# Optimization experiments

Measured on AMD Instinct MI355X. Metric: run time of the kernel, lower is better.

Reference implementation:

```python
import jax, jax.numpy as jnp
import numpy as np
import math

B, T, E, H, L, V = 256, 256, 64, 8, 6, 65
HS = E // H  # head_size = 8


def _pos_encoding():
    position = jnp.arange(T, dtype=jnp.float32)[:, None]
    div_term = jnp.exp(jnp.arange(0, E, 2, dtype=jnp.float32) * (-(math.log(10000.0) / E)))
    pe = jnp.zeros((T, E), dtype=jnp.float32)
    pe = pe.at[:, 0::2].set(jnp.sin(position * div_term))
    pe = pe.at[:, 1::2].set(jnp.cos(position * div_term))
    return pe


def _layernorm(x, g, b, eps=1e-5):
    mu = jnp.mean(x, axis=-1, keepdims=True)
    var = jnp.var(x, axis=-1, keepdims=True)
    return (x - mu) * jax.lax.rsqrt(var + eps) * g + b


def setup_inputs() -> dict:
    key = jax.random.key(0)
    ks = jax.random.split(key, 20)
    s = 0.02
    return {
        "inputs": jax.random.randint(ks[0], (B, T), 0, V),
        "labels": jax.random.randint(ks[1], (B, T), 0, V),
        "emb": jax.random.normal(ks[2], (V, E), jnp.float32) * s,
        "Wq": jax.random.normal(ks[3], (L, E, E), jnp.float32) * s,
        "bq": jnp.zeros((L, E), jnp.float32),
        "Wk": jax.random.normal(ks[4], (L, E, E), jnp.float32) * s,
        "bk": jnp.zeros((L, E), jnp.float32),
        "Wv": jax.random.normal(ks[5], (L, E, E), jnp.float32) * s,
        "bv": jnp.zeros((L, E), jnp.float32),
        "Wo": jax.random.normal(ks[6], (L, E, E), jnp.float32) * s,
        "bo": jnp.zeros((L, E), jnp.float32),
        "ln1_g": jnp.ones((L, E), jnp.float32),
        "ln1_b": jnp.zeros((L, E), jnp.float32),
        "ln2_g": jnp.ones((L, E), jnp.float32),
        "ln2_b": jnp.zeros((L, E), jnp.float32),
        "W1": jax.random.normal(ks[7], (L, E, 4 * E), jnp.float32) * s,
        "b1": jnp.zeros((L, 4 * E), jnp.float32),
        "W2": jax.random.normal(ks[8], (L, 4 * E, E), jnp.float32) * s,
        "b2": jnp.zeros((L, E), jnp.float32),
        "Wout": jax.random.normal(ks[9], (E, V), jnp.float32) * s,
        "bout": jnp.zeros((V,), jnp.float32),
    }


def reference(inputs, labels, emb, Wq, bq, Wk, bk, Wv, bv, Wo, bo,
              ln1_g, ln1_b, ln2_g, ln2_b, W1, b1, W2, b2, Wout, bout):
    x = emb[inputs] + _pos_encoding()[None, :, :]  # [B,T,E]
    causal = jnp.triu(jnp.ones((T, T), dtype=bool), k=1)  # True above diagonal -> masked
    scale = 1.0 / jnp.sqrt(jnp.float32(HS))
    for l in range(L):
        q = (x @ Wq[l] + bq[l]).reshape(B, T, H, HS)
        k = (x @ Wk[l] + bk[l]).reshape(B, T, H, HS)
        v = (x @ Wv[l] + bv[l]).reshape(B, T, H, HS)
        scores = jnp.einsum('bqhd,bkhd->bhqk', q, k) * scale  # [B,H,T,T]
        scores = jnp.where(causal, jnp.float32(-1e9), scores)
        attn = jax.nn.softmax(scores, axis=-1)
        o = jnp.einsum('bhqk,bkhd->bqhd', attn, v).reshape(B, T, E)
        x = _layernorm(x + (o @ Wo[l] + bo[l]), ln1_g[l], ln1_b[l])
        ff = jax.nn.relu(x @ W1[l] + b1[l]) @ W2[l] + b2[l]
        x = _layernorm(x + ff, ln2_g[l], ln2_b[l])
    logits = (x @ Wout + bout).reshape(B * T, V)
    logp = jax.nn.log_softmax(logits, axis=-1)
    loss = -jnp.mean(jnp.take_along_axis(logp, labels.reshape(B * T, 1), axis=-1))
    return logits, loss
```

## Files before the change

### kernel.cpp

```cpp
#include <hip/hip_runtime.h>
#include <math.h>

#define VOCAB 65
#define NBATCH 256

typedef __attribute__((ext_vector_type(8))) short bf16x8;
typedef __attribute__((ext_vector_type(4))) float f32x4;

#define MFMA16(a, b, c) __builtin_amdgcn_mfma_f32_16x16x32_bf16((a), (b), (c), 0, 0, 0)

__device__ __forceinline__ unsigned short f2b(float f) {
    union { float f; unsigned u; } v; v.f = f;
    unsigned r = (v.u + 0x7fffu + ((v.u >> 16) & 1u)) >> 16;
    return (unsigned short)r;
}
__device__ __forceinline__ unsigned cvtpk(float lo, float hi) {
    unsigned r; asm("v_cvt_pk_bf16_f32 %0, %1, %2" : "=v"(r) : "v"(lo), "v"(hi)); return r;
}
__device__ __forceinline__ unsigned short f2b1(float v) { return (unsigned short)cvtpk(v, v); }
__device__ __forceinline__ float b2f(unsigned short h) {
    union { unsigned u; float f; } v; v.u = ((unsigned)h) << 16; return v.f;
}
__device__ __forceinline__ float lo2f(unsigned wd) {
    union { unsigned u; float f; } v; v.u = wd << 16; return v.f;
}
__device__ __forceinline__ float hi2f(unsigned wd) {
    union { unsigned u; float f; } v; v.u = wd & 0xffff0000u; return v.f;
}

__global__ __launch_bounds__(256)
void prep_kernel(const float* __restrict__ Wq, const float* __restrict__ Wk,
                 const float* __restrict__ Wv, const float* __restrict__ Wo,
                 const float* __restrict__ W1, const float* __restrict__ W2,
                 const float* __restrict__ Wout, unsigned short* __restrict__ wbuf) {
    int l = blockIdx.y;
    int idx = blockIdx.x * 256 + threadIdx.x;
    if (l < 6) {
        float v; unsigned short* dst;
        if (idx < 12288) {
            int mat = idx >> 12, m = (idx >> 6) & 63, k = idx & 63;
            const float* W = mat == 0 ? Wq : (mat == 1 ? Wk : Wv);
            v = W[l * 4096 + k * 64 + m];
            dst = wbuf + l * 12288 + idx;
        } else if (idx < 16384) {
            int j = idx - 12288; int m = j >> 6, k = j & 63;
            v = Wo[l * 4096 + k * 64 + m];
            dst = wbuf + 73728 + l * 4096 + j;
        } else if (idx < 32768) {
            int j = idx - 16384; int m = j >> 6, k = j & 63;
            v = W1[l * 16384 + k * 256 + m];
            dst = wbuf + 98304 + l * 16384 + j;
        } else {
            int j = idx - 32768; int m = j >> 8, k = j & 255;
            v = W2[l * 16384 + k * 64 + m];
            dst = wbuf + 196608 + l * 16384 + j;
        }
        *dst = f2b(v);
    } else {
        if (idx < 5120) {
            int m = idx >> 6, k = idx & 63;
            float v = (m < 65) ? Wout[k * 65 + m] : 0.f;
            wbuf[294912 + idx] = f2b(v);
        } else if (idx < 21504) {
            int j = idx - 5120; int t = j >> 6, e = j & 63;
            int i2 = e >> 1;
            float div = expf(-(float)(2 * i2) * 0.14391156831212788f);
            float ang = (float)t * div;
            ((float*)(wbuf + 300032))[j] = (e & 1) ? cosf(ang) : sinf(ang);
        }
    }
}

__global__ __launch_bounds__(512)
void tf_kernel(const int* __restrict__ inp, const int* __restrict__ labels,
               const float* __restrict__ emb,
               const float* __restrict__ bq, const float* __restrict__ bk,
               const float* __restrict__ bv, const float* __restrict__ bo,
               const float* __restrict__ ln1g, const float* __restrict__ ln1b,
               const float* __restrict__ ln2g, const float* __restrict__ ln2b,
               const float* __restrict__ b1, const float* __restrict__ b2,
               const float* __restrict__ bout,
               const unsigned short* __restrict__ wbuf,
               float* __restrict__ out_logits, float* __restrict__ partials) {
    __shared__ __attribute__((aligned(16))) char smem[106528];
    unsigned short (*xb)[72]      = (unsigned short (*)[72])(smem);
    unsigned short (*q2)[24]      = (unsigned short (*)[24])(smem + 36864);
    unsigned short (*k2)[24]      = (unsigned short (*)[24])(smem + 49152);
    unsigned short (*vt)[264]     = (unsigned short (*)[264])(smem + 61440);
    unsigned short (*pcb)[16][40] = (unsigned short (*)[16][40])(smem + 69888);
    unsigned short (*proj)[72]    = (unsigned short (*)[72])(smem + 36864);
    unsigned short (*hb)[136]     = (unsigned short (*)[136])(smem + 36864);
    float* red = (float*)(smem + 106496);

    const unsigned short* wqkvt = wbuf;
    const unsigned short* wot   = wbuf + 73728;
    const unsigned short* w1t   = wbuf + 98304;
    const unsigned short* w2t   = wbuf + 196608;
    const unsigned short* woutt = wbuf + 294912;
    const float* pef = (const float*)(wbuf + 300032);

    const int b = blockIdx.x;
    const int tid = threadIdx.x;
    const int w = tid >> 6;
    const int lane = tid & 63;
    const int cc = lane & 15;
    const int gg = lane >> 4;

    const bf16x8 zf = {0, 0, 0, 0, 0, 0, 0, 0};
    const bf16x8 ones = {(short)0x3F80, (short)0x3F80, (short)0x3F80, (short)0x3F80,
                         (short)0x3F80, (short)0x3F80, (short)0x3F80, (short)0x3F80};

    unsigned rr[16];
    const int lrow = tid >> 1, lq = tid & 1;

    {
        int id = inp[b * 256 + lrow];
        const float4* er = (const float4*)(emb + id * 64 + 32 * lq);
        const float4* pr = (const float4*)(pef + lrow * 64 + 32 * lq);
        #pragma unroll
        for (int j = 0; j < 8; ++j) {
            float4 ev = er[j], pv = pr[j];
            rr[2 * j]     = cvtpk(ev.x + pv.x, ev.y + pv.y);
            rr[2 * j + 1] = cvtpk(ev.z + pv.z, ev.w + pv.w);
        }
        #pragma unroll
        for (int j = 0; j < 4; ++j)
            *(uint4*)&xb[lrow][32 * lq + 8 * j] = make_uint4(rr[4 * j], rr[4 * j + 1], rr[4 * j + 2], rr[4 * j + 3]);
    }
    __syncthreads();

    auto ownerLN = [&](const float* gp_, const float* bp_) {
        unsigned pw[16];
        #pragma unroll
        for (int j = 0; j < 4; ++j) {
            uint4 p = *(const uint4*)&proj[lrow][32 * lq + 8 * j];
            pw[4 * j] = p.x; pw[4 * j + 1] = p.y; pw[4 * j + 2] = p.z; pw[4 * j + 3] = p.w;
        }
        float xv[32];
        float s = 0.f, s2 = 0.f;
        #pragma unroll
        for (int j = 0; j < 16; ++j) {
            float x0 = lo2f(rr[j]) + lo2f(pw[j]);
            float x1 = hi2f(rr[j]) + hi2f(pw[j]);
            xv[2 * j] = x0; xv[2 * j + 1] = x1;
            s += x0 + x1; s2 += x0 * x0 + x1 * x1;
        }
        s  += __shfl_xor(s, 1, 64);
        s2 += __shfl_xor(s2, 1, 64);
        float mu = s * 0.015625f;
        float var = s2 * 0.015625f - mu * mu;
        float rstd = rsqrtf(var + 1e-5f);
        const float4* gp = (const float4*)(gp_ + 32 * lq);
        const float4* bp = (const float4*)(bp_ + 32 * lq);
        #pragma unroll
        for (int j = 0; j < 8; ++j) {
            float4 gv = gp[j], bv2 = bp[j];
            float n0 = (xv[4 * j]     - mu) * rstd * gv.x + bv2.x;
            float n1 = (xv[4 * j + 1] - mu) * rstd * gv.y + bv2.y;
            float n2 = (xv[4 * j + 2] - mu) * rstd * gv.z + bv2.z;
            float n3 = (xv[4 * j + 3] - mu) * rstd * gv.w + bv2.w;
            rr[2 * j]     = cvtpk(n0, n1);
            rr[2 * j + 1] = cvtpk(n2, n3);
        }
        #pragma unroll
        for (int j = 0; j < 4; ++j)
            *(uint4*)&xb[lrow][32 * lq + 8 * j] = make_uint4(rr[4 * j], rr[4 * j + 1], rr[4 * j + 2], rr[4 * j + 3]);
    };

    for (int l = 0; l < 6; ++l) {
        const unsigned short* Wqkv = wqkvt + l * 12288;

        bf16x8 af00 = *(const bf16x8*)&xb[16 * (2 * w)     + cc][8 * gg];
        bf16x8 af01 = *(const bf16x8*)&xb[16 * (2 * w)     + cc][32 + 8 * gg];
        bf16x8 af10 = *(const bf16x8*)&xb[16 * (2 * w + 1) + cc][8 * gg];
        bf16x8 af11 = *(const bf16x8*)&xb[16 * (2 * w + 1) + cc][32 + 8 * gg];

        #pragma unroll
        for (int p = 0; p < 4; ++p) {
            __syncthreads();
            #pragma unroll
            for (int mat = 0; mat < 3; ++mat) {
                const unsigned short* Wt = Wqkv + mat * 4096;
                bf16x8 bf0 = *(const bf16x8*)&Wt[(16 * p + cc) * 64 + 8 * gg];
                bf16x8 bf1 = *(const bf16x8*)&Wt[(16 * p + cc) * 64 + 32 + 8 * gg];
                const float* bias = (mat == 0 ? bq : (mat == 1 ? bk : bv)) + l * 64;
                float bb = bias[16 * p + cc];
                #pragma unroll
                for (int mi = 0; mi < 2; ++mi) {
                    int mt = 2 * w + mi;
                    f32x4 c = {0.f, 0.f, 0.f, 0.f};
                    c = MFMA16(mi ? af10 : af00, bf0, c);
                    c = MFMA16(mi ? af11 : af01, bf1, c);
                    if (mat == 0) {
                        #pragma unroll
                        for (int r = 0; r < 4; ++r)
                            q2[16 * mt + 4 * gg + r][cc] = f2b1((c[r] + bb) * 0.35355339059327373f);
                    } else if (mat == 1) {
                        #pragma unroll
                        for (int r = 0; r < 4; ++r)
                            k2[16 * mt + 4 * gg + r][cc] = f2b1(c[r] + bb);
                    } else {
                        uint2 pk;
                        pk.x = cvtpk(c[0] + bb, c[1] + bb);
                        pk.y = cvtpk(c[2] + bb, c[3] + bb);
                        *(uint2*)&vt[cc][16 * mt + 4 * gg] = pk;
                    }
                }
            }
            __syncthreads();

            #pragma unroll
            for (int hh = 0; hh < 2; ++hh) {
                const int h = 2 * p + hh;
                const int hoff = 8 * hh;
                int a_ = (w + h) & 7;
                #pragma unroll
                for (int s = 0; s < 2; ++s) {
                    int i = s ? (15 - a_) : a_;
                    bf16x8 qf = zf;
                    if (gg == 0) qf = *(const bf16x8*)&q2[16 * i + cc][hoff];
                    f32x4 o = {0.f, 0.f, 0.f, 0.f};
                    int full = i >> 1;
                    for (int jc = 0; jc < full; ++jc) {
                        #pragma unroll
                        for (int jt2 = 0; jt2 < 2; ++jt2) {
                            int jt = 2 * jc + jt2;
                            bf16x8 kf = zf;
                            if (gg == 0) kf = *(const bf16x8*)&k2[16 * jt + cc][hoff];
                            f32x4 sc = {0.f, 0.f, 0.f, 0.f};
                            sc = MFMA16(kf, qf, sc);
                            uint2 pk;
                            pk.x = cvtpk(__expf(sc[0]), __expf(sc[1]));
                            pk.y = cvtpk(__expf(sc[2]), __expf(sc[3]));
                            *(uint2*)&pcb[w][cc][16 * jt2 + 4 * gg] = pk;
                        }
                        asm volatile("" ::: "memory");
                        bf16x8 pa = *(const bf16x8*)&pcb[w][cc][8 * gg];
                        bf16x8 vb;
                        if (cc < 8)       vb = *(const bf16x8*)&vt[hoff + cc][32 * jc + 8 * gg];
                        else if (cc == 8) vb = ones;
                        else              vb = zf;
                        o = MFMA16(pa, vb, o);
                        asm volatile("" ::: "memory");
                    }
                    {
                        int jc = full;
                        #pragma unroll
                        for (int jt2 = 0; jt2 < 2; ++jt2) {
                            int jt = 2 * jc + jt2;
                            uint2 pk = make_uint2(0u, 0u);
                            if (jt <= i) {
                                bf16x8 kf = zf;
                                if (gg == 0) kf = *(const bf16x8*)&k2[16 * jt + cc][hoff];
                                f32x4 sc = {0.f, 0.f, 0.f, 0.f};
                                sc = MFMA16(kf, qf, sc);
                                float pv[4];
                                #pragma unroll
                                for (int r = 0; r < 4; ++r) {
                                    float pp = __expf(sc[r]);
                                    if (jt == i && 4 * gg + r > cc) pp = 0.f;
                                    pv[r] = pp;
                                }
                                pk.x = cvtpk(pv[0], pv[1]);
                                pk.y = cvtpk(pv[2], pv[3]);
                            }
                            *(uint2*)&pcb[w][cc][16 * jt2 + 4 * gg] = pk;
                        }
                        asm volatile("" ::: "memory");
                        bf16x8 pa = *(const bf16x8*)&pcb[w][cc][8 * gg];
                        bf16x8 vb;
                        if (cc < 8)       vb = *(const bf16x8*)&vt[hoff + cc][32 * jc + 8 * gg];
                        else if (cc == 8) vb = ones;
                        else              vb = zf;
                        o = MFMA16(pa, vb, o);
                        asm volatile("" ::: "memory");
                    }
                    #pragma unroll
                    for (int r = 0; r < 4; ++r) {
                        float rs = __shfl(o[r], (lane & 48) + 8, 64);
                        float ov = o[r] * __builtin_amdgcn_rcpf(rs);
                        if (cc < 8)
                            xb[16 * i + 4 * gg + r][8 * h + cc] = f2b1(ov);
                    }
                }
            }
        }
        __syncthreads();

        {
            const unsigned short* Wt = wot + l * 4096;
            int n = w & 3;
            bf16x8 bf0 = *(const bf16x8*)&Wt[(16 * n + cc) * 64 + 8 * gg];
            bf16x8 bf1 = *(const bf16x8*)&Wt[(16 * n + cc) * 64 + 32 + 8 * gg];
            float bb = bo[l * 64 + 16 * n + cc];
            #pragma unroll
            for (int mi = 0; mi < 8; ++mi) {
                int mt = 8 * (w >> 2) + mi;
                bf16x8 o0 = *(const bf16x8*)&xb[16 * mt + cc][8 * gg];
                bf16x8 o1 = *(const bf16x8*)&xb[16 * mt + cc][32 + 8 * gg];
                f32x4 c = {0.f, 0.f, 0.f, 0.f};
                c = MFMA16(o0, bf0, c);
                c = MFMA16(o1, bf1, c);
                #pragma unroll
                for (int r = 0; r < 4; ++r)
                    proj[16 * mt + 4 * gg + r][16 * n + cc] = f2b1(c[r] + bb);
            }
        }
        __syncthreads();
        ownerLN(ln1g + l * 64, ln1b + l * 64);
        __syncthreads();

        f32x4 facc[8];
        #pragma unroll
        for (int t = 0; t < 8; ++t) facc[t] = {0.f, 0.f, 0.f, 0.f};
        #pragma unroll
        for (int ch = 0; ch < 2; ++ch) {
            if (ch) __syncthreads();
            {
                const unsigned short* Wt = w1t + l * 16384;
                int gcol = 128 * ch + 16 * w + cc;
                bf16x8 bf0 = *(const bf16x8*)&Wt[gcol * 64 + 8 * gg];
                bf16x8 bf1 = *(const bf16x8*)&Wt[gcol * 64 + 32 + 8 * gg];
                float bb = b1[l * 256 + gcol];
                #pragma unroll
                for (int mt = 0; mt < 16; ++mt) {
                    bf16x8 x0 = *(const bf16x8*)&xb[16 * mt + cc][8 * gg];
                    bf16x8 x1 = *(const bf16x8*)&xb[16 * mt + cc][32 + 8 * gg];
                    f32x4 c = {0.f, 0.f, 0.f, 0.f};
                    c = MFMA16(x0, bf0, c);
                    c = MFMA16(x1, bf1, c);
                    #pragma unroll
                    for (int r = 0; r < 4; ++r)
                        hb[16 * mt + 4 * gg + r][16 * w + cc] = f2b1(fmaxf(c[r] + bb, 0.f));
                }
            }
            __syncthreads();
            {
                const unsigned short* Wt = w2t + l * 16384;
                int n = w & 3;
                #pragma unroll
                for (int ks = 0; ks < 4; ++ks) {
                    bf16x8 bf0 = *(const bf16x8*)&Wt[(16 * n + cc) * 256 + 128 * ch + 32 * ks + 8 * gg];
                    #pragma unroll
                    for (int mi = 0; mi < 8; ++mi) {
                        int mt = 8 * (w >> 2) + mi;
                        bf16x8 h0 = *(const bf16x8*)&hb[16 * mt + cc][32 * ks + 8 * gg];
                        facc[mi] = MFMA16(h0, bf0, facc[mi]);
                    }
                }
            }
        }
        __syncthreads();
        {
            int n = w & 3;
            float bb = b2[l * 64 + 16 * n + cc];
            #pragma unroll
            for (int mi = 0; mi < 8; ++mi) {
                int mt = 8 * (w >> 2) + mi;
                #pragma unroll
                for (int r = 0; r < 4; ++r)
                    proj[16 * mt + 4 * gg + r][16 * n + cc] = f2b1(facc[mi][r] + bb);
            }
        }
        __syncthreads();
        ownerLN(ln2g + l * 64, ln2b + l * 64);
        __syncthreads();
    }

    #pragma unroll
    for (int t = 0; t < 10; ++t) {
        int id = w + 8 * t;
        int n = id >> 4, mt = id & 15;
        bf16x8 a0 = *(const bf16x8*)&xb[16 * mt + cc][8 * gg];
        bf16x8 a1 = *(const bf16x8*)&xb[16 * mt + cc][32 + 8 * gg];
        bf16x8 bf0 = *(const bf16x8*)&woutt[(16 * n + cc) * 64 + 8 * gg];
        bf16x8 bf1 = *(const bf16x8*)&woutt[(16 * n + cc) * 64 + 32 + 8 * gg];
        f32x4 c = {0.f, 0.f, 0.f, 0.f};
        c = MFMA16(a0, bf0, c);
        c = MFMA16(a1, bf1, c);
        int col = 16 * n + cc;
        if (col < 65) {
            float bb = bout[col];
            #pragma unroll
            for (int r = 0; r < 4; ++r) {
                int row = 16 * mt + 4 * gg + r;
                float v = c[r] + bb;
                out_logits[((size_t)b * 256 + row) * 65 + col] = v;
                proj[row][col] = f2b1(v);
            }
        }
    }
    __syncthreads();

    {
        float sum = 0.f;
        for (int c2 = lq; c2 < 65; c2 += 2) sum += __expf(b2f(proj[lrow][c2]));
        sum += __shfl_xor(sum, 1, 64);
        float nll = 0.f;
        if (lq == 0) {
            int lab = labels[b * 256 + lrow];
            nll = logf(sum) - b2f(proj[lrow][lab]);
        }
        #pragma unroll
        for (int m = 1; m < 64; m <<= 1) nll += __shfl_xor(nll, m, 64);
        if (lane == 0) red[w] = nll;
        __syncthreads();
        if (tid == 0) {
            float s = 0.f;
            #pragma unroll
            for (int i = 0; i < 8; ++i) s += red[i];
            partials[b] = s;
        }
    }
}

__global__ __launch_bounds__(64)
void loss_reduce(const float* __restrict__ partials, float* __restrict__ out) {
    int t = threadIdx.x;
    float s = partials[t] + partials[t + 64] + partials[t + 128] + partials[t + 192];
    #pragma unroll
    for (int m = 1; m < 64; m <<= 1) s += __shfl_xor(s, m, 64);
    if (t == 0) out[0] = s * (1.f / 65536.f);
}

extern "C" void kernel_launch(void* const* d_in, const int* in_sizes, int n_in,
                              void* d_out, int out_size, void* d_ws, size_t ws_size,
                              hipStream_t stream) {
    const int*   inputs = (const int*)d_in[0];
    const int*   labels = (const int*)d_in[1];
    const float* emb  = (const float*)d_in[2];
    const float* Wq   = (const float*)d_in[3];
    const float* bq   = (const float*)d_in[4];
    const float* Wk   = (const float*)d_in[5];
    const float* bk   = (const float*)d_in[6];
    const float* Wv   = (const float*)d_in[7];
    const float* bv   = (const float*)d_in[8];
    const float* Wo   = (const float*)d_in[9];
    const float* bo   = (const float*)d_in[10];
    const float* ln1g = (const float*)d_in[11];
    const float* ln1b = (const float*)d_in[12];
    const float* ln2g = (const float*)d_in[13];
    const float* ln2b = (const float*)d_in[14];
    const float* W1   = (const float*)d_in[15];
    const float* b1   = (const float*)d_in[16];
    const float* W2   = (const float*)d_in[17];
    const float* b2   = (const float*)d_in[18];
    const float* Wout = (const float*)d_in[19];
    const float* bout = (const float*)d_in[20];

    float* logits = (float*)d_out;
    float* loss   = logits + (size_t)65536 * 65;

    float* partials = (float*)d_ws;
    unsigned short* wbuf = (unsigned short*)((char*)d_ws + 1024);

    prep_kernel<<<dim3(192, 7), 256, 0, stream>>>(Wq, Wk, Wv, Wo, W1, W2, Wout, wbuf);
    tf_kernel<<<NBATCH, 512, 0, stream>>>(inputs, labels, emb,
                                          bq, bk, bv, bo,
                                          ln1g, ln1b, ln2g, ln2b,
                                          b1, b2, bout,
                                          wbuf, logits, partials);
    loss_reduce<<<1, 64, 0, stream>>>(partials, loss);
}
```

Baseline: 309.7 us.

## Process four heads per QKV phase and double-chunk attention inner loop

QKV projection now produces 32 columns (four heads) per phase instead of 16, halving the number of projection/attention phases and block-wide barriers per layer. The attention inner loop processes two 32-key chunks per iteration into separate accumulators, so the score MFMAs and exp work of two chunks can overlap before the P·V MFMAs. This also merges the full-chunk and diagonal-chunk paths into one masked path. The cost is more LDS (larger q/k/v/pcb buffers), extra masking checks on every chunk, and more register pressure.

```diff
diff --git a/kernel.cpp b/kernel.cpp
--- a/kernel.cpp
+++ b/kernel.cpp
@@ -82,15 +82,15 @@
                const float* __restrict__ bout,
                const unsigned short* __restrict__ wbuf,
                float* __restrict__ out_logits, float* __restrict__ partials) {
-    __shared__ __attribute__((aligned(16))) char smem[106528];
+    __shared__ __attribute__((aligned(16))) char smem[113184];
     unsigned short (*xb)[72]      = (unsigned short (*)[72])(smem);
-    unsigned short (*q2)[24]      = (unsigned short (*)[24])(smem + 36864);
-    unsigned short (*k2)[24]      = (unsigned short (*)[24])(smem + 49152);
-    unsigned short (*vt)[264]     = (unsigned short (*)[264])(smem + 61440);
-    unsigned short (*pcb)[16][40] = (unsigned short (*)[16][40])(smem + 69888);
+    unsigned short (*q2)[40]      = (unsigned short (*)[40])(smem + 36864);
+    unsigned short (*k2)[40]      = (unsigned short (*)[40])(smem + 57344);
+    unsigned short (*vt)[264]     = (unsigned short (*)[264])(smem + 77824);
+    unsigned short (*pcb)[16][72] = (unsigned short (*)[16][72])(smem + 94720);
     unsigned short (*proj)[72]    = (unsigned short (*)[72])(smem + 36864);
     unsigned short (*hb)[136]     = (unsigned short (*)[136])(smem + 36864);
-    float* red = (float*)(smem + 106496);
+    float* red = (float*)(smem + 113152);
 
     const unsigned short* wqkvt = wbuf;
     const unsigned short* wot   = wbuf + 73728;
@@ -176,82 +176,64 @@
         bf16x8 af11 = *(const bf16x8*)&xb[16 * (2 * w + 1) + cc][32 + 8 * gg];
 
         #pragma unroll
-        for (int p = 0; p < 4; ++p) {
-            __syncthreads();
-            #pragma unroll
-            for (int mat = 0; mat < 3; ++mat) {
-                const unsigned short* Wt = Wqkv + mat * 4096;
-                bf16x8 bf0 = *(const bf16x8*)&Wt[(16 * p + cc) * 64 + 8 * gg];
-                bf16x8 bf1 = *(const bf16x8*)&Wt[(16 * p + cc) * 64 + 32 + 8 * gg];
-                const float* bias = (mat == 0 ? bq : (mat == 1 ? bk : bv)) + l * 64;
-                float bb = bias[16 * p + cc];
-                #pragma unroll
-                for (int mi = 0; mi < 2; ++mi) {
-                    int mt = 2 * w + mi;
-                    f32x4 c = {0.f, 0.f, 0.f, 0.f};
-                    c = MFMA16(mi ? af10 : af00, bf0, c);
-                    c = MFMA16(mi ? af11 : af01, bf1, c);
-                    if (mat == 0) {
-                        #pragma unroll
-                        for (int r = 0; r < 4; ++r)
-                            q2[16 * mt + 4 * gg + r][cc] = f2b1((c[r] + bb) * 0.35355339059327373f);
-                    } else if (mat == 1) {
-                        #pragma unroll
-                        for (int r = 0; r < 4; ++r)
-                            k2[16 * mt + 4 * gg + r][cc] = f2b1(c[r] + bb);
-                    } else {
-                        uint2 pk;
-                        pk.x = cvtpk(c[0] + bb, c[1] + bb);
-                        pk.y = cvtpk(c[2] + bb, c[3] + bb);
-                        *(uint2*)&vt[cc][16 * mt + 4 * gg] = pk;
+        for (int ph = 0; ph < 2; ++ph) {
+            if (ph) __syncthreads();
+            #pragma unroll
+            for (int lp = 0; lp < 2; ++lp) {
+                const int p = 2 * ph + lp;
+                #pragma unroll
+                for (int mat = 0; mat < 3; ++mat) {
+                    const unsigned short* Wt = Wqkv + mat * 4096;
+                    bf16x8 bf0 = *(const bf16x8*)&Wt[(16 * p + cc) * 64 + 8 * gg];
+                    bf16x8 bf1 = *(const bf16x8*)&Wt[(16 * p + cc) * 64 + 32 + 8 * gg];
+                    const float* bias = (mat == 0 ? bq : (mat == 1 ? bk : bv)) + l * 64;
+                    float bb = bias[16 * p + cc];
+                    #pragma unroll
+                    for (int mi = 0; mi < 2; ++mi) {
+                        int mt = 2 * w + mi;
+                        f32x4 c = {0.f, 0.f, 0.f, 0.f};
+                        c = MFMA16(mi ? af10 : af00, bf0, c);
+                        c = MFMA16(mi ? af11 : af01, bf1, c);
+                        if (mat == 0) {
+                            #pragma unroll
+                            for (int r = 0; r < 4; ++r)
+                                q2[16 * mt + 4 * gg + r][16 * lp + cc] = f2b1((c[r] + bb) * 0.35355339059327373f);
+                        } else if (mat == 1) {
+                            #pragma unroll
+                            for (int r = 0; r < 4; ++r)
+                                k2[16 * mt + 4 * gg + r][16 * lp + cc] = f2b1(c[r] + bb);
+                        } else {
+                            uint2 pk;
+                            pk.x = cvtpk(c[0] + bb, c[1] + bb);
+                            pk.y = cvtpk(c[2] + bb, c[3] + bb);
+                            *(uint2*)&vt[16 * lp + cc][16 * mt + 4 * gg] = pk;
+                        }
                     }
                 }
             }
             __syncthreads();
 
             #pragma unroll
-            for (int hh = 0; hh < 2; ++hh) {
-                const int h = 2 * p + hh;
-                const int hoff = 8 * hh;
+            for (int hh = 0; hh < 4; ++hh) {
+                const int h = 4 * ph + hh;
+                const int ho = 8 * hh;
                 int a_ = (w + h) & 7;
                 #pragma unroll
                 for (int s = 0; s < 2; ++s) {
                     int i = s ? (15 - a_) : a_;
                     bf16x8 qf = zf;
-                    if (gg == 0) qf = *(const bf16x8*)&q2[16 * i + cc][hoff];
-                    f32x4 o = {0.f, 0.f, 0.f, 0.f};
-                    int full = i >> 1;
-                    for (int jc = 0; jc < full; ++jc) {
+                    if (gg == 0) qf = *(const bf16x8*)&q2[16 * i + cc][ho];
+                    f32x4 o0 = {0.f, 0.f, 0.f, 0.f}, o1 = {0.f, 0.f, 0.f, 0.f};
+                    const int full = i >> 1;
+
+                    auto prod = [&](int c, int stc) {
                         #pragma unroll
                         for (int jt2 = 0; jt2 < 2; ++jt2) {
-                            int jt = 2 * jc + jt2;
-                            bf16x8 kf = zf;
-                            if (gg == 0) kf = *(const bf16x8*)&k2[16 * jt + cc][hoff];
-                            f32x4 sc = {0.f, 0.f, 0.f, 0.f};
-                            sc = MFMA16(kf, qf, sc);
-                            uint2 pk;
-                            pk.x = cvtpk(__expf(sc[0]), __expf(sc[1]));
-                            pk.y = cvtpk(__expf(sc[2]), __expf(sc[3]));
-                            *(uint2*)&pcb[w][cc][16 * jt2 + 4 * gg] = pk;
-                        }
-                        asm volatile("" ::: "memory");
-                        bf16x8 pa = *(const bf16x8*)&pcb[w][cc][8 * gg];
-                        bf16x8 vb;
-                        if (cc < 8)       vb = *(const bf16x8*)&vt[hoff + cc][32 * jc + 8 * gg];
-                        else if (cc == 8) vb = ones;
-                        else              vb = zf;
-                        o = MFMA16(pa, vb, o);
-                        asm volatile("" ::: "memory");
-                    }
-                    {
-                        int jc = full;
-                        #pragma unroll
-                        for (int jt2 = 0; jt2 < 2; ++jt2) {
-                            int jt = 2 * jc + jt2;
+                            int jt = 2 * c + jt2;
                             uint2 pk = make_uint2(0u, 0u);
                             if (jt <= i) {
                                 bf16x8 kf = zf;
-                                if (gg == 0) kf = *(const bf16x8*)&k2[16 * jt + cc][hoff];
+                                if (gg == 0) kf = *(const bf16x8*)&k2[16 * jt + cc][ho];
                                 f32x4 sc = {0.f, 0.f, 0.f, 0.f};
                                 sc = MFMA16(kf, qf, sc);
                                 float pv[4];
@@ -264,21 +246,33 @@
                                 pk.x = cvtpk(pv[0], pv[1]);
                                 pk.y = cvtpk(pv[2], pv[3]);
                             }
-                            *(uint2*)&pcb[w][cc][16 * jt2 + 4 * gg] = pk;
+                            *(uint2*)&pcb[w][cc][stc + 16 * jt2 + 4 * gg] = pk;
                         }
-                        asm volatile("" ::: "memory");
-                        bf16x8 pa = *(const bf16x8*)&pcb[w][cc][8 * gg];
+                    };
+                    auto cons = [&](int c, int stc, f32x4& o) {
+                        bf16x8 pa = *(const bf16x8*)&pcb[w][cc][stc + 8 * gg];
                         bf16x8 vb;
-                        if (cc < 8)       vb = *(const bf16x8*)&vt[hoff + cc][32 * jc + 8 * gg];
+                        if (cc < 8)       vb = *(const bf16x8*)&vt[ho + cc][32 * c + 8 * gg];
                         else if (cc == 8) vb = ones;
                         else              vb = zf;
                         o = MFMA16(pa, vb, o);
+                    };
+
+                    for (int j2 = 0; 2 * j2 <= full; ++j2) {
+                        int cA = 2 * j2, cB = 2 * j2 + 1;
+                        bool hasB = (cB <= full);
+                        prod(cA, 0);
+                        if (hasB) prod(cB, 32);
+                        asm volatile("" ::: "memory");
+                        cons(cA, 0, o0);
+                        if (hasB) cons(cB, 32, o1);
                         asm volatile("" ::: "memory");
                     }
                     #pragma unroll
                     for (int r = 0; r < 4; ++r) {
-                        float rs = __shfl(o[r], (lane & 48) + 8, 64);
-                        float ov = o[r] * __builtin_amdgcn_rcpf(rs);
+                        float ov = o0[r] + o1[r];
+                        float rs = __shfl(ov, (lane & 48) + 8, 64);
+                        ov = ov * __builtin_amdgcn_rcpf(rs);
                         if (cc < 8)
                             xb[16 * i + 4 * gg + r][8 * h + cc] = f2b1(ov);
                     }
```

Result: slower. 339.8 us (+9.7%).

## Compute full QKV once per layer and run all heads without per-pair barriers

Applied to the files above, without the earlier changes.

The QKV projection is now computed for all four head pairs up front into full-width q/k/v shared buffers, followed by a single barrier. Attention then loops over all eight heads with no intermediate __syncthreads. The per-wave probability buffer is double-windowed by alternating 32-column halves, and the compiler memory fences between stores and loads are removed. This roughly doubles the shared-memory footprint (about 163KB), which still allows one block per CU but risks LDS capacity limits. It also relies on implicit in-wave ordering for the P-buffer reuse.

```diff
diff --git a/kernel.cpp b/kernel.cpp
--- a/kernel.cpp
+++ b/kernel.cpp
@@ -82,15 +82,15 @@
                const float* __restrict__ bout,
                const unsigned short* __restrict__ wbuf,
                float* __restrict__ out_logits, float* __restrict__ partials) {
-    __shared__ __attribute__((aligned(16))) char smem[106528];
+    __shared__ __attribute__((aligned(16))) char smem[162848];
     unsigned short (*xb)[72]      = (unsigned short (*)[72])(smem);
-    unsigned short (*q2)[24]      = (unsigned short (*)[24])(smem + 36864);
-    unsigned short (*k2)[24]      = (unsigned short (*)[24])(smem + 49152);
-    unsigned short (*vt)[264]     = (unsigned short (*)[264])(smem + 61440);
-    unsigned short (*pcb)[16][40] = (unsigned short (*)[16][40])(smem + 69888);
+    unsigned short (*q2)[72]      = (unsigned short (*)[72])(smem + 36864);
+    unsigned short (*k2)[72]      = (unsigned short (*)[72])(smem + 73728);
+    unsigned short (*vt)[264]     = (unsigned short (*)[264])(smem + 110592);
+    unsigned short (*pcb)[16][72] = (unsigned short (*)[16][72])(smem + 144384);
     unsigned short (*proj)[72]    = (unsigned short (*)[72])(smem + 36864);
     unsigned short (*hb)[136]     = (unsigned short (*)[136])(smem + 36864);
-    float* red = (float*)(smem + 106496);
+    float* red = (float*)(smem + 162816);
 
     const unsigned short* wqkvt = wbuf;
     const unsigned short* wot   = wbuf + 73728;
@@ -177,7 +177,6 @@
 
         #pragma unroll
         for (int p = 0; p < 4; ++p) {
-            __syncthreads();
             #pragma unroll
             for (int mat = 0; mat < 3; ++mat) {
                 const unsigned short* Wt = Wqkv + mat * 4096;
@@ -194,94 +193,91 @@
                     if (mat == 0) {
                         #pragma unroll
                         for (int r = 0; r < 4; ++r)
-                            q2[16 * mt + 4 * gg + r][cc] = f2b1((c[r] + bb) * 0.35355339059327373f);
+                            q2[16 * mt + 4 * gg + r][16 * p + cc] = f2b1((c[r] + bb) * 0.35355339059327373f);
                     } else if (mat == 1) {
                         #pragma unroll
                         for (int r = 0; r < 4; ++r)
-                            k2[16 * mt + 4 * gg + r][cc] = f2b1(c[r] + bb);
+                            k2[16 * mt + 4 * gg + r][16 * p + cc] = f2b1(c[r] + bb);
                     } else {
                         uint2 pk;
                         pk.x = cvtpk(c[0] + bb, c[1] + bb);
                         pk.y = cvtpk(c[2] + bb, c[3] + bb);
-                        *(uint2*)&vt[cc][16 * mt + 4 * gg] = pk;
+                        *(uint2*)&vt[16 * p + cc][16 * mt + 4 * gg] = pk;
                     }
                 }
             }
-            __syncthreads();
-
-            #pragma unroll
-            for (int hh = 0; hh < 2; ++hh) {
-                const int h = 2 * p + hh;
-                const int hoff = 8 * hh;
-                int a_ = (w + h) & 7;
-                #pragma unroll
-                for (int s = 0; s < 2; ++s) {
-                    int i = s ? (15 - a_) : a_;
-                    bf16x8 qf = zf;
-                    if (gg == 0) qf = *(const bf16x8*)&q2[16 * i + cc][hoff];
-                    f32x4 o = {0.f, 0.f, 0.f, 0.f};
-                    int full = i >> 1;
-                    for (int jc = 0; jc < full; ++jc) {
-                        #pragma unroll
-                        for (int jt2 = 0; jt2 < 2; ++jt2) {
-                            int jt = 2 * jc + jt2;
+        }
+        __syncthreads();
+
+        #pragma unroll
+        for (int h = 0; h < 8; ++h) {
+            const int ho = 8 * h;
+            int a_ = (w + h) & 7;
+            #pragma unroll
+            for (int s = 0; s < 2; ++s) {
+                int i = s ? (15 - a_) : a_;
+                bf16x8 qf = zf;
+                if (gg == 0) qf = *(const bf16x8*)&q2[16 * i + cc][ho];
+                f32x4 o = {0.f, 0.f, 0.f, 0.f};
+                int full = i >> 1;
+                for (int jc = 0; jc < full; ++jc) {
+                    int win = (jc & 1) * 32;
+                    #pragma unroll
+                    for (int jt2 = 0; jt2 < 2; ++jt2) {
+                        int jt = 2 * jc + jt2;
+                        bf16x8 kf = zf;
+                        if (gg == 0) kf = *(const bf16x8*)&k2[16 * jt + cc][ho];
+                        f32x4 sc = {0.f, 0.f, 0.f, 0.f};
+                        sc = MFMA16(kf, qf, sc);
+                        uint2 pk;
+                        pk.x = cvtpk(__expf(sc[0]), __expf(sc[1]));
+                        pk.y = cvtpk(__expf(sc[2]), __expf(sc[3]));
+                        *(uint2*)&pcb[w][cc][win + 16 * jt2 + 4 * gg] = pk;
+                    }
+                    bf16x8 pa = *(const bf16x8*)&pcb[w][cc][win + 8 * gg];
+                    bf16x8 vb;
+                    if (cc < 8)       vb = *(const bf16x8*)&vt[ho + cc][32 * jc + 8 * gg];
+                    else if (cc == 8) vb = ones;
+                    else              vb = zf;
+                    o = MFMA16(pa, vb, o);
+                }
+                {
+                    int jc = full;
+                    int win = (full & 1) * 32;
+                    #pragma unroll
+                    for (int jt2 = 0; jt2 < 2; ++jt2) {
+                        int jt = 2 * jc + jt2;
+                        uint2 pk = make_uint2(0u, 0u);
+                        if (jt <= i) {
                             bf16x8 kf = zf;
-                            if (gg == 0) kf = *(const bf16x8*)&k2[16 * jt + cc][hoff];
+                            if (gg == 0) kf = *(const bf16x8*)&k2[16 * jt + cc][ho];
                             f32x4 sc = {0.f, 0.f, 0.f, 0.f};
                             sc = MFMA16(kf, qf, sc);
-                            uint2 pk;
-                            pk.x = cvtpk(__expf(sc[0]), __expf(sc[1]));
-                            pk.y = cvtpk(__expf(sc[2]), __expf(sc[3]));
-                            *(uint2*)&pcb[w][cc][16 * jt2 + 4 * gg] = pk;
+                            float pv[4];
+                            #pragma unroll
+                            for (int r = 0; r < 4; ++r) {
+                                float pp = __expf(sc[r]);
+                                if (jt == i && 4 * gg + r > cc) pp = 0.f;
+                                pv[r] = pp;
+                            }
+                            pk.x = cvtpk(pv[0], pv[1]);
+                            pk.y = cvtpk(pv[2], pv[3]);
                         }
-                        asm volatile("" ::: "memory");
-                        bf16x8 pa = *(const bf16x8*)&pcb[w][cc][8 * gg];
-                        bf16x8 vb;
-                        if (cc < 8)       vb = *(const bf16x8*)&vt[hoff + cc][32 * jc + 8 * gg];
-                        else if (cc == 8) vb = ones;
-                        else              vb = zf;
-                        o = MFMA16(pa, vb, o);
-                        asm volatile("" ::: "memory");
+                        *(uint2*)&pcb[w][cc][win + 16 * jt2 + 4 * gg] = pk;
                     }
-                    {
-                        int jc = full;
-                        #pragma unroll
-                        for (int jt2 = 0; jt2 < 2; ++jt2) {
-                            int jt = 2 * jc + jt2;
-                            uint2 pk = make_uint2(0u, 0u);
-                            if (jt <= i) {
-                                bf16x8 kf = zf;
-                                if (gg == 0) kf = *(const bf16x8*)&k2[16 * jt + cc][hoff];
-                                f32x4 sc = {0.f, 0.f, 0.f, 0.f};
-                                sc = MFMA16(kf, qf, sc);
-                                float pv[4];
-                                #pragma unroll
-                                for (int r = 0; r < 4; ++r) {
-                                    float pp = __expf(sc[r]);
-                                    if (jt == i && 4 * gg + r > cc) pp = 0.f;
-                                    pv[r] = pp;
-                                }
-                                pk.x = cvtpk(pv[0], pv[1]);
-                                pk.y = cvtpk(pv[2], pv[3]);
-                            }
-                            *(uint2*)&pcb[w][cc][16 * jt2 + 4 * gg] = pk;
-                        }
-                        asm volatile("" ::: "memory");
-                        bf16x8 pa = *(const bf16x8*)&pcb[w][cc][8 * gg];
-                        bf16x8 vb;
-                        if (cc < 8)       vb = *(const bf16x8*)&vt[hoff + cc][32 * jc + 8 * gg];
-                        else if (cc == 8) vb = ones;
-                        else              vb = zf;
-                        o = MFMA16(pa, vb, o);
-                        asm volatile("" ::: "memory");
-                    }
-                    #pragma unroll
-                    for (int r = 0; r < 4; ++r) {
-                        float rs = __shfl(o[r], (lane & 48) + 8, 64);
-                        float ov = o[r] * __builtin_amdgcn_rcpf(rs);
-                        if (cc < 8)
-                            xb[16 * i + 4 * gg + r][8 * h + cc] = f2b1(ov);
-                    }
+                    bf16x8 pa = *(const bf16x8*)&pcb[w][cc][win + 8 * gg];
+                    bf16x8 vb;
+                    if (cc < 8)       vb = *(const bf16x8*)&vt[ho + cc][32 * jc + 8 * gg];
+                    else if (cc == 8) vb = ones;
+                    else              vb = zf;
+                    o = MFMA16(pa, vb, o);
+                }
+                #pragma unroll
+                for (int r = 0; r < 4; ++r) {
+                    float rs = __shfl(o[r], (lane & 48) + 8, 64);
+                    float ov = o[r] * __builtin_amdgcn_rcpf(rs);
+                    if (cc < 8)
+                        xb[16 * i + 4 * gg + r][ho + cc] = f2b1(ov);
                 }
             }
         }
```

New measurement: 334.1 us. 7.9% more time.
